# Optimization experiments

Measured on AMD Instinct MI355X. Metric: run time of the kernel, lower is better.

The kernel has to match this reference:

```python
import jax, jax.numpy as jnp
import numpy as np

N = 8192      # nodes
F = 256       # input feature dim
D_OUT = 256   # output_dim


def setup_inputs() -> dict:
    key = jax.random.key(0)
    k1, k2, k3 = jax.random.split(key, 3)
    data = jax.random.normal(k1, (1, N, F), dtype=jnp.float32)
    # dense (normalized) adjacency; the original converts dense->sparse then matmuls,
    # which is mathematically a dense adj @ data product.
    adj = jax.random.uniform(k2, (1, N, N), dtype=jnp.float32)
    kernel = jax.random.normal(k3, (F, D_OUT), dtype=jnp.float32)
    return {"data": data, "adj": adj, "kernel": kernel}


def reference(data, adj, kernel):
    # af = adj @ data  : [N, N] @ [N, F] -> [N, F]  (neighbor aggregation)
    af = jnp.matmul(adj[0], data[0])
    # dense projection: [N, F] @ [F, D_OUT] -> [N, D_OUT]
    out = jnp.matmul(af, kernel)
    # expand batch dim back and apply activation (relu)
    return jax.nn.relu(out[None, :, :])
```

## Files before the change

kernel.cpp:

```cpp
#include <hip/hip_runtime.h>
#include <stdint.h>

#define AS1 __attribute__((address_space(1)))
#define AS3 __attribute__((address_space(3)))

typedef float f32x4 __attribute__((ext_vector_type(4)));
typedef __bf16 bf16x8 __attribute__((ext_vector_type(8)));
typedef uint32_t u32x2 __attribute__((ext_vector_type(2)));

__device__ __forceinline__ unsigned short f2bf(float f) {
    uint32_t x = __float_as_uint(f);
    x += 0x7FFFu + ((x >> 16) & 1u);
    return (unsigned short)(x >> 16);
}

__device__ __forceinline__ void gload_lds16(const void* g, void* l) {
    __builtin_amdgcn_global_load_lds((const AS1 void*)g, (AS3 void*)l, 16, 0, 0);
}

__global__ __launch_bounds__(256) void wt_kernel(const float* __restrict__ W,
                                                 unsigned short* __restrict__ WT) {
    __shared__ float tile[32][33];
    const int bf = blockIdx.x & 7;
    const int bn = blockIdx.x >> 3;
    const int t = threadIdx.x;
    const int c = t & 31, r = t >> 5;
#pragma unroll
    for (int i = 0; i < 4; ++i)
        tile[r + i * 8][c] = W[(bf * 32 + r + i * 8) * 256 + bn * 32 + c];
    __syncthreads();
#pragma unroll
    for (int i = 0; i < 4; ++i)
        WT[(bn * 32 + r + i * 8) * 256 + bf * 32 + c] = f2bf(tile[c][r + i * 8]);
}

template <int LDA, int LDB, int KSTEPS>
__global__ __launch_bounds__(256) void gemm1_kernel(const float* __restrict__ A,
                                                    const unsigned short* __restrict__ B,
                                                    unsigned short* __restrict__ dkT) {
    __shared__ unsigned short Alds[32 * 64];
    __shared__ unsigned short Blds[256 * 64];

    const int t = threadIdx.x;
    const int w = t >> 6;
    const int l = t & 63;
    const int m0 = blockIdx.x * 32;

    const int ar = t >> 3;
    const int kq = t & 7;
    const float* gA = A + (size_t)(m0 + ar) * LDA + kq * 4;
    char* aw0 = (char*)Alds + ((ar * 128 + kq * 8) ^ ((ar & 7) << 4));
    char* aw1 = (char*)Alds + ((ar * 128 + 64 + kq * 8) ^ ((ar & 7) << 4));

    const int nr_base = w * 64 + (l >> 3);
    const int c16 = l & 7;

    f32x4 acc[2][4];
#pragma unroll
    for (int i = 0; i < 2; ++i)
#pragma unroll
        for (int j = 0; j < 4; ++j) acc[i][j] = (f32x4){0.f, 0.f, 0.f, 0.f};

    for (int step = 0; step < KSTEPS; ++step) {
        const int k0 = step * 64;
        __syncthreads();
#pragma unroll
        for (int i = 0; i < 8; ++i) {
            const int nr = nr_base + i * 8;
            const unsigned short* src =
                B + (size_t)nr * LDB + k0 + ((c16 ^ (nr & 7)) << 3);
            gload_lds16(src, (char*)Blds + (w * 512 + i * 64) * 16);
        }
        const f32x4 v0 = *(const f32x4*)(gA + k0);
        const f32x4 v1 = *(const f32x4*)(gA + k0 + 32);
        uint32_t p0 = (uint32_t)f2bf(v0.x) | ((uint32_t)f2bf(v0.y) << 16);
        uint32_t p1 = (uint32_t)f2bf(v0.z) | ((uint32_t)f2bf(v0.w) << 16);
        uint32_t p2 = (uint32_t)f2bf(v1.x) | ((uint32_t)f2bf(v1.y) << 16);
        uint32_t p3 = (uint32_t)f2bf(v1.z) | ((uint32_t)f2bf(v1.w) << 16);
        ((uint32_t*)aw0)[0] = p0;
        ((uint32_t*)aw0)[1] = p1;
        ((uint32_t*)aw1)[0] = p2;
        ((uint32_t*)aw1)[1] = p3;
        __syncthreads();
#pragma unroll
        for (int kh = 0; kh < 2; ++kh) {
            const int koffb = kh * 64 + ((l >> 4) << 4);
            bf16x8 af[2], bv[4];
#pragma unroll
            for (int im = 0; im < 2; ++im) {
                const int r = im * 16 + (l & 15);
                af[im] = *(const bf16x8*)((const char*)Alds +
                                          ((r * 128 + koffb) ^ ((r & 7) << 4)));
            }
#pragma unroll
            for (int jn = 0; jn < 4; ++jn) {
                const int n = w * 64 + jn * 16 + (l & 15);
                bv[jn] = *(const bf16x8*)((const char*)Blds +
                                          ((n * 128 + koffb) ^ ((n & 7) << 4)));
            }
#pragma unroll
            for (int im = 0; im < 2; ++im)
#pragma unroll
                for (int jn = 0; jn < 4; ++jn)
                    acc[im][jn] = __builtin_amdgcn_mfma_f32_16x16x32_bf16(
                        af[im], bv[jn], acc[im][jn], 0, 0, 0);
        }
    }

#pragma unroll
    for (int im = 0; im < 2; ++im) {
        const int mb = m0 + im * 16 + ((l >> 4) << 2);
#pragma unroll
        for (int jn = 0; jn < 4; ++jn) {
            const int n = w * 64 + jn * 16 + (l & 15);
            const uint32_t lo = (uint32_t)f2bf(acc[im][jn][0]) |
                                ((uint32_t)f2bf(acc[im][jn][1]) << 16);
            const uint32_t hi = (uint32_t)f2bf(acc[im][jn][2]) |
                                ((uint32_t)f2bf(acc[im][jn][3]) << 16);
            uint32_t* dst = (uint32_t*)&dkT[(size_t)n * 8192 + mb];
            dst[0] = lo;
            dst[1] = hi;
        }
    }
}

template <int KSPLIT>
__global__ __launch_bounds__(256, 3) void gemm2_kernel(const float* __restrict__ A,
                                                       const unsigned short* __restrict__ B,
                                                       float* __restrict__ Out0,
                                                       float* __restrict__ Pws) {
    __shared__ unsigned short Alds[64 * 64];
    __shared__ unsigned short Blds[256 * 64];

    const int t = threadIdx.x;
    const int w = t >> 6;
    const int l = t & 63;
    const int mtile = blockIdx.x / KSPLIT;
    const int ks = blockIdx.x % KSPLIT;
    const int m0 = mtile * 64;
    const int kbase = ks * (8192 / KSPLIT);
    constexpr int KSTEPS = (8192 / KSPLIT) / 64;

    const int jr = t >> 4;
    const int jc = t & 15;
    const float* gA = A + (size_t)(m0 + jr) * 8192 + kbase + jc * 4;

    const int nr_base = w * 64 + (l >> 3);
    const int c16 = l & 7;

    f32x4 acc[4][4];
#pragma unroll
    for (int i = 0; i < 4; ++i)
#pragma unroll
        for (int j = 0; j < 4; ++j) acc[i][j] = (f32x4){0.f, 0.f, 0.f, 0.f};

    const int q = l >> 4;
    const int li = l & 15;

    for (int step = 0; step < KSTEPS; ++step) {
        const int k0 = step * 64;
        __syncthreads();
#pragma unroll
        for (int i = 0; i < 8; ++i) {
            const int nr = nr_base + i * 8;
            const unsigned short* src =
                B + (size_t)nr * 8192 + kbase + k0 + ((c16 ^ (nr & 7)) << 3);
            gload_lds16(src, (char*)Blds + (w * 512 + i * 64) * 16);
        }
#pragma unroll
        for (int j = 0; j < 4; ++j) {
            const f32x4 v = *(const f32x4*)(gA + (size_t)j * 16 * 8192 + k0);
            const int r = j * 16 + jr;
            const int p = (jc >> 1) ^ (r & 7);
            u32x2 pk;
            pk[0] = (uint32_t)f2bf(v.x) | ((uint32_t)f2bf(v.y) << 16);
            pk[1] = (uint32_t)f2bf(v.z) | ((uint32_t)f2bf(v.w) << 16);
            *(u32x2*)((char*)Alds + r * 128 + p * 16 + (jc & 1) * 8) = pk;
        }
        __syncthreads();
#pragma unroll
        for (int kh = 0; kh < 2; ++kh) {
            const int koffb = kh * 64 + (q << 4);
            bf16x8 af[4], bv[4];
#pragma unroll
            for (int im = 0; im < 4; ++im) {
                const int r = im * 16 + li;
                af[im] = *(const bf16x8*)((const char*)Alds +
                                          ((r * 128 + koffb) ^ ((r & 7) << 4)));
            }
#pragma unroll
            for (int jn = 0; jn < 4; ++jn) {
                const int n = w * 64 + jn * 16 + li;
                bv[jn] = *(const bf16x8*)((const char*)Blds +
                                          ((n * 128 + koffb) ^ ((n & 7) << 4)));
            }
#pragma unroll
            for (int im = 0; im < 4; ++im)
#pragma unroll
                for (int jn = 0; jn < 4; ++jn)
                    acc[im][jn] = __builtin_amdgcn_mfma_f32_16x16x32_bf16(
                        af[im], bv[jn], acc[im][jn], 0, 0, 0);
        }
    }

    float* Og = (KSPLIT == 1 || ks == 0) ? Out0
                                         : (Pws + (size_t)(ks - 1) * (8192 * 256));
#pragma unroll
    for (int im = 0; im < 4; ++im) {
        const int row0 = m0 + im * 16 + (q << 2);
#pragma unroll
        for (int jn = 0; jn < 4; ++jn) {
            const int col = w * 64 + jn * 16 + li;
#pragma unroll
            for (int r = 0; r < 4; ++r) {
                float v = acc[im][jn][r];
                if (KSPLIT == 1) v = v > 0.f ? v : 0.f;
                Og[(size_t)(row0 + r) * 256 + col] = v;
            }
        }
    }
}

template <int S>
__global__ __launch_bounds__(256) void reduce_relu_kernel(float* __restrict__ out,
                                                          const float* __restrict__ P) {
    const int i = blockIdx.x * 256 + threadIdx.x;
    f32x4 v = ((const f32x4*)out)[i];
#pragma unroll
    for (int s = 0; s < S - 1; ++s) {
        const f32x4 p = ((const f32x4*)P)[(size_t)s * 524288 + i];
        v.x += p.x; v.y += p.y; v.z += p.z; v.w += p.w;
    }
    v.x = v.x > 0.f ? v.x : 0.f;
    v.y = v.y > 0.f ? v.y : 0.f;
    v.z = v.z > 0.f ? v.z : 0.f;
    v.w = v.w > 0.f ? v.w : 0.f;
    ((f32x4*)out)[i] = v;
}

extern "C" void kernel_launch(void* const* d_in, const int* in_sizes, int n_in,
                              void* d_out, int out_size, void* d_ws, size_t ws_size,
                              hipStream_t stream) {
    const float* data = (const float*)d_in[0];
    const float* adj = (const float*)d_in[1];
    const float* Wk = (const float*)d_in[2];
    float* out = (float*)d_out;

    unsigned short* WT = (unsigned short*)d_ws;
    unsigned short* dkT = (unsigned short*)((char*)d_ws + 131072);
    float* P = (float*)((char*)d_ws + 131072 + 4194304);

    const size_t base_need = 131072 + 4194304;
    const size_t part_bytes = (size_t)8192 * 256 * 4;

    wt_kernel<<<64, 256, 0, stream>>>(Wk, WT);
    gemm1_kernel<256, 256, 4><<<256, 256, 0, stream>>>(data, WT, dkT);
    if (ws_size >= base_need + 7 * part_bytes) {
        gemm2_kernel<8><<<1024, 256, 0, stream>>>(adj, dkT, out, P);
        reduce_relu_kernel<8><<<2048, 256, 0, stream>>>(out, P);
    } else if (ws_size >= base_need + part_bytes) {
        gemm2_kernel<2><<<256, 256, 0, stream>>>(adj, dkT, out, P);
        reduce_relu_kernel<2><<<2048, 256, 0, stream>>>(out, P);
    } else {
        gemm2_kernel<1><<<128, 256, 0, stream>>>(adj, dkT, out, nullptr);
    }
}
```

Measured before the change: 111.3 us.

## Enlarge gemm2 tile to 128 rows with 512 threads and store bf16 split-K partials

The adjacency GEMM block grows from 64x256 to 128x256 with 8 waves arranged 2x4, so each B (dkT) tile loaded into LDS is reused across twice as many adj rows, halving B traffic per row. Split-K partials are now written as bf16 into separate slices, and the reduction kernel sums all slices, including slice 0, in fp32 before applying ReLU. This halves partial write and read bytes in exchange for rounding error in the partial sums, plus higher LDS use and register pressure per block.

```diff
diff --git a/kernel.cpp b/kernel.cpp
--- a/kernel.cpp
+++ b/kernel.cpp
@@ -7,11 +7,16 @@
 typedef float f32x4 __attribute__((ext_vector_type(4)));
 typedef __bf16 bf16x8 __attribute__((ext_vector_type(8)));
 typedef uint32_t u32x2 __attribute__((ext_vector_type(2)));
+typedef unsigned short u16;
+typedef u16 u16x8 __attribute__((ext_vector_type(8)));
 
 __device__ __forceinline__ unsigned short f2bf(float f) {
     uint32_t x = __float_as_uint(f);
     x += 0x7FFFu + ((x >> 16) & 1u);
     return (unsigned short)(x >> 16);
+}
+__device__ __forceinline__ float bf2f(unsigned short u) {
+    return __uint_as_float((uint32_t)u << 16);
 }
 
 __device__ __forceinline__ void gload_lds16(const void* g, void* l) {
@@ -125,57 +130,57 @@
 }
 
 template <int KSPLIT>
-__global__ __launch_bounds__(256, 3) void gemm2_kernel(const float* __restrict__ A,
+__global__ __launch_bounds__(512, 6) void gemm2_kernel(const float* __restrict__ A,
                                                        const unsigned short* __restrict__ B,
                                                        float* __restrict__ Out0,
-                                                       float* __restrict__ Pws) {
-    __shared__ unsigned short Alds[64 * 64];
+                                                       u16* __restrict__ Pws) {
+    __shared__ unsigned short Alds[128 * 64];
     __shared__ unsigned short Blds[256 * 64];
 
     const int t = threadIdx.x;
     const int w = t >> 6;
     const int l = t & 63;
+    const int wr = w >> 2;
+    const int wc = w & 3;
+    const int q = l >> 4;
+    const int li = l & 15;
     const int mtile = blockIdx.x / KSPLIT;
     const int ks = blockIdx.x % KSPLIT;
-    const int m0 = mtile * 64;
+    const int m0 = mtile * 128;
     const int kbase = ks * (8192 / KSPLIT);
     constexpr int KSTEPS = (8192 / KSPLIT) / 64;
 
-    const int jr = t >> 4;
+    const int rr0 = t >> 4;
     const int jc = t & 15;
-    const float* gA = A + (size_t)(m0 + jr) * 8192 + kbase + jc * 4;
-
-    const int nr_base = w * 64 + (l >> 3);
-    const int c16 = l & 7;
+    const float* gA = A + (size_t)(m0 + rr0) * 8192 + kbase + jc * 4;
+    const int ap = (jc >> 1) ^ (rr0 & 7);
+    char* const awbase = (char*)Alds + rr0 * 128 + ap * 16 + (jc & 1) * 8;
+
+    const int br0 = t >> 3;
+    const int c16 = t & 7;
+    const unsigned short* gB =
+        B + (size_t)br0 * 8192 + kbase + ((c16 ^ (br0 & 7)) << 3);
 
     f32x4 acc[4][4];
 #pragma unroll
     for (int i = 0; i < 4; ++i)
 #pragma unroll
         for (int j = 0; j < 4; ++j) acc[i][j] = (f32x4){0.f, 0.f, 0.f, 0.f};
-
-    const int q = l >> 4;
-    const int li = l & 15;
 
     for (int step = 0; step < KSTEPS; ++step) {
         const int k0 = step * 64;
         __syncthreads();
 #pragma unroll
-        for (int i = 0; i < 8; ++i) {
-            const int nr = nr_base + i * 8;
-            const unsigned short* src =
-                B + (size_t)nr * 8192 + kbase + k0 + ((c16 ^ (nr & 7)) << 3);
-            gload_lds16(src, (char*)Blds + (w * 512 + i * 64) * 16);
-        }
+        for (int i = 0; i < 4; ++i)
+            gload_lds16(gB + (size_t)i * 64 * 8192 + k0,
+                        (char*)Blds + (i * 512 + w * 64) * 16);
 #pragma unroll
         for (int j = 0; j < 4; ++j) {
-            const f32x4 v = *(const f32x4*)(gA + (size_t)j * 16 * 8192 + k0);
-            const int r = j * 16 + jr;
-            const int p = (jc >> 1) ^ (r & 7);
+            const f32x4 v = *(const f32x4*)(gA + (size_t)j * 32 * 8192 + k0);
             u32x2 pk;
             pk[0] = (uint32_t)f2bf(v.x) | ((uint32_t)f2bf(v.y) << 16);
             pk[1] = (uint32_t)f2bf(v.z) | ((uint32_t)f2bf(v.w) << 16);
-            *(u32x2*)((char*)Alds + r * 128 + p * 16 + (jc & 1) * 8) = pk;
+            *(u32x2*)(awbase + j * 32 * 128) = pk;
         }
         __syncthreads();
 #pragma unroll
@@ -184,13 +189,13 @@
             bf16x8 af[4], bv[4];
 #pragma unroll
             for (int im = 0; im < 4; ++im) {
-                const int r = im * 16 + li;
+                const int r = wr * 64 + im * 16 + li;
                 af[im] = *(const bf16x8*)((const char*)Alds +
                                           ((r * 128 + koffb) ^ ((r & 7) << 4)));
             }
 #pragma unroll
             for (int jn = 0; jn < 4; ++jn) {
-                const int n = w * 64 + jn * 16 + li;
+                const int n = wc * 64 + jn * 16 + li;
                 bv[jn] = *(const bf16x8*)((const char*)Blds +
                                           ((n * 128 + koffb) ^ ((n & 7) << 4)));
             }
@@ -203,19 +208,31 @@
         }
     }
 
-    float* Og = (KSPLIT == 1 || ks == 0) ? Out0
-                                         : (Pws + (size_t)(ks - 1) * (8192 * 256));
-#pragma unroll
-    for (int im = 0; im < 4; ++im) {
-        const int row0 = m0 + im * 16 + (q << 2);
-#pragma unroll
-        for (int jn = 0; jn < 4; ++jn) {
-            const int col = w * 64 + jn * 16 + li;
-#pragma unroll
-            for (int r = 0; r < 4; ++r) {
-                float v = acc[im][jn][r];
-                if (KSPLIT == 1) v = v > 0.f ? v : 0.f;
-                Og[(size_t)(row0 + r) * 256 + col] = v;
+    if (KSPLIT == 1) {
+#pragma unroll
+        for (int im = 0; im < 4; ++im) {
+            const int row0 = m0 + wr * 64 + im * 16 + (q << 2);
+#pragma unroll
+            for (int jn = 0; jn < 4; ++jn) {
+                const int col = wc * 64 + jn * 16 + li;
+#pragma unroll
+                for (int r = 0; r < 4; ++r) {
+                    const float v = acc[im][jn][r];
+                    Out0[(size_t)(row0 + r) * 256 + col] = v > 0.f ? v : 0.f;
+                }
+            }
+        }
+    } else {
+        u16* Pb = Pws + (size_t)ks * (8192 * 256);
+#pragma unroll
+        for (int im = 0; im < 4; ++im) {
+            const int row0 = m0 + wr * 64 + im * 16 + (q << 2);
+#pragma unroll
+            for (int jn = 0; jn < 4; ++jn) {
+                const int col = wc * 64 + jn * 16 + li;
+#pragma unroll
+                for (int r = 0; r < 4; ++r)
+                    Pb[(size_t)(row0 + r) * 256 + col] = f2bf(acc[im][jn][r]);
             }
         }
     }
@@ -223,19 +240,22 @@
 
 template <int S>
 __global__ __launch_bounds__(256) void reduce_relu_kernel(float* __restrict__ out,
-                                                          const float* __restrict__ P) {
-    const int i = blockIdx.x * 256 + threadIdx.x;
-    f32x4 v = ((const f32x4*)out)[i];
-#pragma unroll
-    for (int s = 0; s < S - 1; ++s) {
-        const f32x4 p = ((const f32x4*)P)[(size_t)s * 524288 + i];
-        v.x += p.x; v.y += p.y; v.z += p.z; v.w += p.w;
-    }
-    v.x = v.x > 0.f ? v.x : 0.f;
-    v.y = v.y > 0.f ? v.y : 0.f;
-    v.z = v.z > 0.f ? v.z : 0.f;
-    v.w = v.w > 0.f ? v.w : 0.f;
-    ((f32x4*)out)[i] = v;
+                                                          const u16* __restrict__ P) {
+    const size_t i = (size_t)blockIdx.x * 256 + threadIdx.x;
+    float s0 = 0, s1 = 0, s2 = 0, s3 = 0, s4 = 0, s5 = 0, s6 = 0, s7 = 0;
+#pragma unroll
+    for (int s = 0; s < S; ++s) {
+        const u16x8 v = ((const u16x8*)(P + (size_t)s * (8192 * 256)))[i];
+        s0 += bf2f(v[0]); s1 += bf2f(v[1]); s2 += bf2f(v[2]); s3 += bf2f(v[3]);
+        s4 += bf2f(v[4]); s5 += bf2f(v[5]); s6 += bf2f(v[6]); s7 += bf2f(v[7]);
+    }
+    f32x4 lo, hi;
+    lo.x = s0 > 0.f ? s0 : 0.f; lo.y = s1 > 0.f ? s1 : 0.f;
+    lo.z = s2 > 0.f ? s2 : 0.f; lo.w = s3 > 0.f ? s3 : 0.f;
+    hi.x = s4 > 0.f ? s4 : 0.f; hi.y = s5 > 0.f ? s5 : 0.f;
+    hi.z = s6 > 0.f ? s6 : 0.f; hi.w = s7 > 0.f ? s7 : 0.f;
+    ((f32x4*)out)[2 * i] = lo;
+    ((f32x4*)out)[2 * i + 1] = hi;
 }
 
 extern "C" void kernel_launch(void* const* d_in, const int* in_sizes, int n_in,
@@ -248,20 +268,20 @@
 
     unsigned short* WT = (unsigned short*)d_ws;
     unsigned short* dkT = (unsigned short*)((char*)d_ws + 131072);
-    float* P = (float*)((char*)d_ws + 131072 + 4194304);
+    u16* Pb = (u16*)((char*)d_ws + 131072 + 4194304);
 
     const size_t base_need = 131072 + 4194304;
-    const size_t part_bytes = (size_t)8192 * 256 * 4;
+    const size_t part_bytes = (size_t)8192 * 256 * 2;
 
     wt_kernel<<<64, 256, 0, stream>>>(Wk, WT);
     gemm1_kernel<256, 256, 4><<<256, 256, 0, stream>>>(data, WT, dkT);
-    if (ws_size >= base_need + 7 * part_bytes) {
-        gemm2_kernel<8><<<1024, 256, 0, stream>>>(adj, dkT, out, P);
-        reduce_relu_kernel<8><<<2048, 256, 0, stream>>>(out, P);
-    } else if (ws_size >= base_need + part_bytes) {
-        gemm2_kernel<2><<<256, 256, 0, stream>>>(adj, dkT, out, P);
-        reduce_relu_kernel<2><<<2048, 256, 0, stream>>>(out, P);
+    if (ws_size >= base_need + 8 * part_bytes) {
+        gemm2_kernel<8><<<512, 512, 0, stream>>>(adj, dkT, out, Pb);
+        reduce_relu_kernel<8><<<1024, 256, 0, stream>>>(out, Pb);
+    } else if (ws_size >= base_need + 2 * part_bytes) {
+        gemm2_kernel<2><<<128, 512, 0, stream>>>(adj, dkT, out, Pb);
+        reduce_relu_kernel<2><<<1024, 256, 0, stream>>>(out, Pb);
     } else {
-        gemm2_kernel<1><<<128, 256, 0, stream>>>(adj, dkT, out, nullptr);
-    }
-}
+        gemm2_kernel<1><<<64, 512, 0, stream>>>(adj, dkT, out, nullptr);
+    }
+}
```

Measured after the change: 246.5 us. 122% more time.
